# Kernel optimization log

Hardware: AMD Instinct MI355X
Metric: run time of the kernel (lower is better)

## Reference

```python
import jax, jax.numpy as jnp
import numpy as np

D_MODEL, D_STATE, D_CONV, EXPAND = 1024, 16, 4, 2
D_INNER = D_MODEL * EXPAND
B, T = 1, 2048
EPS = 1e-5


def setup_inputs() -> dict:
    key = jax.random.key(0)
    ks = jax.random.split(key, 8)
    x = jax.random.normal(ks[0], (B, T, D_MODEL), dtype=jnp.float32)
    W_in = jax.random.normal(ks[1], (D_MODEL, 2 * D_INNER), dtype=jnp.float32) * 0.02
    conv_w = jax.random.normal(ks[2], (D_INNER, D_CONV), dtype=jnp.float32) * 0.2
    conv_b = jax.random.normal(ks[3], (D_INNER,), dtype=jnp.float32) * 0.02
    W_x = jax.random.normal(ks[4], (D_INNER, 2 * D_STATE + 1), dtype=jnp.float32) * 0.02
    W_dt = jax.random.normal(ks[5], (1, D_INNER), dtype=jnp.float32) * 0.5
    b_dt = jax.random.uniform(ks[6], (D_INNER,), dtype=jnp.float32, minval=-0.001, maxval=0.001)
    A_log = jnp.broadcast_to(jnp.log(jnp.arange(1, D_STATE + 1, dtype=jnp.float32))[None, :], (D_INNER, D_STATE))
    Dparam = jnp.ones((D_INNER,), dtype=jnp.float32)
    W_out = jax.random.normal(ks[7], (D_INNER, D_MODEL), dtype=jnp.float32) * 0.02
    ln_g = jnp.ones((D_MODEL,), dtype=jnp.float32)
    ln_b = jnp.zeros((D_MODEL,), dtype=jnp.float32)
    return {"x": x, "W_in": W_in, "conv_w": conv_w, "conv_b": conv_b, "W_x": W_x,
            "W_dt": W_dt, "b_dt": b_dt, "A_log": A_log, "D": Dparam,
            "W_out": W_out, "ln_g": ln_g, "ln_b": ln_b}


def _silu(v):
    return v * jax.nn.sigmoid(v)


def _layernorm(v, g, b):
    mu = jnp.mean(v, axis=-1, keepdims=True)
    var = jnp.mean((v - mu) ** 2, axis=-1, keepdims=True)
    return (v - mu) * jax.lax.rsqrt(var + EPS) * g + b


def _causal_depthwise_conv(xp, conv_w, conv_b):
    # xp: (B, T, D_INNER) -> (B, D_INNER, T) with left pad of D_CONV-1
    xc = jnp.swapaxes(xp, 1, 2)
    xc = jnp.pad(xc, ((0, 0), (0, 0), (D_CONV - 1, 0)))
    w = conv_w[:, None, :]  # (O=D_INNER, I/groups=1, K)
    out = jax.lax.conv_general_dilated(
        xc, w, window_strides=(1,), padding='VALID',
        dimension_numbers=('NCH', 'OIH', 'NCH'), feature_group_count=D_INNER)
    return jnp.swapaxes(out + conv_b[None, :, None], 1, 2)  # (B, T, D_INNER)


def reference(x, W_in, conv_w, conv_b, W_x, W_dt, b_dt, A_log, D, W_out, ln_g, ln_b):
    residual = x
    xn = _layernorm(x, ln_g, ln_b)
    xz = xn @ W_in                      # (B, T, 2*D_INNER)
    x_proj, z = jnp.split(xz, 2, axis=-1)
    x_conv = _silu(_causal_depthwise_conv(x_proj, conv_w, conv_b))  # (B, T, D_INNER)

    ssm = x_conv @ W_x                  # (B, T, 1 + 2*D_STATE)
    dt_raw = ssm[..., :1]
    Bp = ssm[..., 1:1 + D_STATE]        # (B, T, D_STATE)
    Cp = ssm[..., 1 + D_STATE:]         # (B, T, D_STATE)
    dt = jax.nn.softplus(dt_raw @ W_dt + b_dt)  # (B, T, D_INNER)

    A = -jnp.exp(A_log)                 # (D_INNER, D_STATE)
    A_bar = jnp.exp(dt[..., None] * A)                              # (B,T,d,n)
    Bx = dt[..., None] * Bp[:, :, None, :] * x_conv[..., None]      # (B,T,d,n)

    def step(h, inp):
        Ab_t, Bx_t, C_t = inp           # (B,d,n),(B,d,n),(B,n)
        h = Ab_t * h + Bx_t
        y_t = jnp.einsum('bdn,bn->bd', h, C_t)
        return h, y_t

    h0 = jnp.zeros((x.shape[0], D_INNER, D_STATE), dtype=x.dtype)
    _, ys = jax.lax.scan(step, h0, (jnp.swapaxes(A_bar, 0, 1),
                                    jnp.swapaxes(Bx, 0, 1),
                                    jnp.swapaxes(Cp, 0, 1)))
    y = jnp.swapaxes(ys, 0, 1)          # (B, T, D_INNER)

    y = y + x_conv * D
    y = y * _silu(z)
    return y @ W_out + residual
```

## Files before the change

### kernel.cpp

```cpp
#include <hip/hip_runtime.h>
#include <hip/hip_bf16.h>

typedef __hip_bfloat16 bf16;
typedef __attribute__((ext_vector_type(8))) short bf16x8;
typedef __attribute__((ext_vector_type(4))) float f32x4;

#define T_LEN 2048
#define DMODEL 1024
#define DINNER 2048
#define DSTATE 16
#define LN_EPS 1e-5f
#define NCHUNK 128
#define CLEN 16
#define SSTR 64

#define GLOBAL_AS __attribute__((address_space(1)))
#define LDS_AS __attribute__((address_space(3)))

__device__ __forceinline__ void g2l16(void* lds, const void* g) {
    __builtin_amdgcn_global_load_lds((const GLOBAL_AS void*)g, (LDS_AS void*)lds, 16, 0, 0);
}

__global__ void transpose_bf16(const float* __restrict__ W, bf16* __restrict__ Wt,
                               int K, int N) {
    __shared__ float t[32][33];
    int n0 = blockIdx.x * 32, k0 = blockIdx.y * 32;
    int tx = threadIdx.x & 31, ty4 = (threadIdx.x >> 5) * 4;
#pragma unroll
    for (int r = 0; r < 4; r++)
        t[ty4 + r][tx] = W[(size_t)(k0 + ty4 + r) * N + n0 + tx];
    __syncthreads();
#pragma unroll
    for (int r = 0; r < 4; r++)
        Wt[(size_t)(n0 + ty4 + r) * K + k0 + tx] = __float2bfloat16(t[tx][ty4 + r]);
}

__global__ void transpose_wx(const float* __restrict__ W, bf16* __restrict__ Wt) {
    int idx = blockIdx.x * 256 + threadIdx.x;
    int n = idx >> 11, k = idx & 2047;
    Wt[idx] = __float2bfloat16(n < 33 ? W[k * 33 + n] : 0.f);
}

__global__ void ln_kernel(const float* __restrict__ x, const float* __restrict__ g,
                          const float* __restrict__ b, bf16* __restrict__ xn) {
    int row = blockIdx.x;
    int tid = threadIdx.x;
    const float* xr = x + (size_t)row * DMODEL;
    float v[4];
    float s = 0.f, q = 0.f;
#pragma unroll
    for (int i = 0; i < 4; i++) {
        v[i] = xr[tid + i * 256];
        s += v[i];
        q += v[i] * v[i];
    }
    __shared__ float sh_s[256], sh_q[256];
    sh_s[tid] = s; sh_q[tid] = q;
    __syncthreads();
    for (int st = 128; st > 0; st >>= 1) {
        if (tid < st) { sh_s[tid] += sh_s[tid + st]; sh_q[tid] += sh_q[tid + st]; }
        __syncthreads();
    }
    float mean = sh_s[0] * (1.f / DMODEL);
    float var  = sh_q[0] * (1.f / DMODEL) - mean * mean;
    float rstd = rsqrtf(var + LN_EPS);
#pragma unroll
    for (int i = 0; i < 4; i++) {
        int c = tid + i * 256;
        xn[(size_t)row * DMODEL + c] = __float2bfloat16((v[i] - mean) * rstd * g[c] + b[c]);
    }
}

template <int BM, int BN, int WAVE_M, int WAVE_N, int WRITE_RESID, int OUT_BF16>
__global__ void gemm_mfma(const bf16* __restrict__ A, const bf16* __restrict__ Bt,
                          void* __restrict__ Cv, const float* __restrict__ resid,
                          int M, int N, int Kslice, int lda) {
    constexpr int WMsz = BM / WAVE_M;
    constexpr int WNsz = BN / WAVE_N;
    constexpr int TM = WMsz / 16;
    constexpr int TN = WNsz / 16;
    __shared__ short As[BM * 64];
    __shared__ short Bs[BN * 64];
    int tid = threadIdx.x;
    int lane = tid & 63, wave = tid >> 6;
    int wm = (wave / WAVE_N) * WMsz, wn = (wave % WAVE_N) * WNsz;
    int rowBase = blockIdx.y * BM, colBase = blockIdx.x * BN;
    int kbase = blockIdx.z * Kslice;

    f32x4 acc[TM][TN];
#pragma unroll
    for (int i = 0; i < TM; i++)
#pragma unroll
        for (int j = 0; j < TN; j++) acc[i][j] = f32x4{0.f, 0.f, 0.f, 0.f};

    int srow = tid >> 3;
    int cc = (tid & 7) ^ (srow & 7);
    const int ldsoff = tid * 16;

    for (int k0 = kbase; k0 < kbase + Kslice; k0 += 64) {
#pragma unroll
        for (int j = 0; j < BM / 32; j++)
            g2l16((char*)As + j * 4096 + ldsoff,
                  A + (size_t)(rowBase + j * 32 + srow) * lda + k0 + cc * 8);
#pragma unroll
        for (int j = 0; j < BN / 32; j++)
            g2l16((char*)Bs + j * 4096 + ldsoff,
                  Bt + (size_t)(colBase + j * 32 + srow) * lda + k0 + cc * 8);
        __syncthreads();
#pragma unroll
        for (int ks = 0; ks < 2; ks++) {
            bf16x8 af[TM], bfr[TN];
#pragma unroll
            for (int i = 0; i < TM; i++) {
                int row = wm + i * 16 + (lane & 15);
                int slot = (ks * 4 + (lane >> 4)) ^ (row & 7);
                af[i] = *(const bf16x8*)((const char*)As + row * 128 + slot * 16);
            }
#pragma unroll
            for (int j = 0; j < TN; j++) {
                int row = wn + j * 16 + (lane & 15);
                int slot = (ks * 4 + (lane >> 4)) ^ (row & 7);
                bfr[j] = *(const bf16x8*)((const char*)Bs + row * 128 + slot * 16);
            }
#pragma unroll
            for (int i = 0; i < TM; i++)
#pragma unroll
                for (int j = 0; j < TN; j++)
                    acc[i][j] = __builtin_amdgcn_mfma_f32_16x16x32_bf16(
                        af[i], bfr[j], acc[i][j], 0, 0, 0);
        }
        __syncthreads();
    }
    int rq = lane >> 4, cn = lane & 15;
    float* Cf = (float*)Cv + (size_t)blockIdx.z * M * N;
#pragma unroll
    for (int i = 0; i < TM; i++) {
#pragma unroll
        for (int j = 0; j < TN; j++) {
#pragma unroll
            for (int r = 0; r < 4; r++) {
                size_t row = rowBase + wm + i * 16 + rq * 4 + r;
                int col = colBase + wn + j * 16 + cn;
                float v = acc[i][j][r];
                if (WRITE_RESID) v += resid[row * N + col];
                if (OUT_BF16)
                    ((bf16*)Cv)[row * N + col] = __float2bfloat16(v);
                else
                    Cf[row * N + col] = v;
            }
        }
    }
}

__global__ void reduce_ssm(const float* __restrict__ parts, float* __restrict__ ssm) {
    int i = blockIdx.x * 256 + threadIdx.x;
    ssm[i] = parts[i] + parts[i + 131072] + parts[i + 2 * 131072] + parts[i + 3 * 131072];
}

__global__ void conv_silu(const bf16* __restrict__ xz, const float* __restrict__ cw,
                          const float* __restrict__ cb, bf16* __restrict__ xc) {
    int idx = blockIdx.x * 256 + threadIdx.x;
    int t = idx >> 11, d = idx & (DINNER - 1);
    float acc = cb[d];
#pragma unroll
    for (int k = 0; k < 4; k++) {
        int tt = t - 3 + k;
        if (tt >= 0) acc += (float)xz[(size_t)tt * (2 * DINNER) + d] * cw[d * 4 + k];
    }
    xc[idx] = __float2bfloat16(acc / (1.f + __expf(-acc)));
}

__device__ __forceinline__ float softplus_f(float pre) {
    return (pre > 20.f) ? pre : log1pf(__expf(pre));
}

__device__ __forceinline__ void powtree(float q, float* a) {
    a[0] = q;
    a[1] = q * q;
    a[2] = a[1] * q;
    a[3] = a[1] * a[1];
#pragma unroll
    for (int j = 0; j < 4; j++) a[4 + j] = a[j] * a[3];
#pragma unroll
    for (int j = 0; j < 8; j++) a[8 + j] = a[j] * a[7];
}

__global__ __launch_bounds__(256, 4) void scan_pass1(
        const float* __restrict__ ssm, const bf16* __restrict__ xc,
        const float* __restrict__ Wdt, const float* __restrict__ bdt,
        const float* __restrict__ Alog,
        float* __restrict__ P, float* __restrict__ S) {
    int d = blockIdx.x * 256 + threadIdx.x;
    int c = blockIdx.y;
    float A[DSTATE], Pv[DSTATE], Sv[DSTATE];
    bool fast = true;
#pragma unroll
    for (int n = 0; n < DSTATE; n++) {
        A[n] = -__expf(Alog[d * DSTATE + n]);
        fast = fast && (fabsf(A[n] + (float)(n + 1)) < 1e-3f * (n + 1));
        Pv[n] = 1.f; Sv[n] = 0.f;
    }
    float wdt = Wdt[d], bd = bdt[d];
    int t0 = c * CLEN;
    if (fast) {
        for (int t = t0; t < t0 + CLEN; t++) {
            const float* srow = ssm + (size_t)t * SSTR;
            float dt = softplus_f(srow[0] * wdt + bd);
            float dtxc = dt * (float)xc[(size_t)t * DINNER + d];
            float a[DSTATE];
            powtree(__expf(-dt), a);
#pragma unroll
            for (int n = 0; n < DSTATE; n++) {
                Pv[n] *= a[n];
                Sv[n] = a[n] * Sv[n] + dtxc * srow[1 + n];
            }
        }
    } else {
        for (int t = t0; t < t0 + CLEN; t++) {
            const float* srow = ssm + (size_t)t * SSTR;
            float dt = softplus_f(srow[0] * wdt + bd);
            float dtxc = dt * (float)xc[(size_t)t * DINNER + d];
#pragma unroll
            for (int n = 0; n < DSTATE; n++) {
                float a = __expf(dt * A[n]);
                Pv[n] *= a;
                Sv[n] = a * Sv[n] + dtxc * srow[1 + n];
            }
        }
    }
    size_t base = (size_t)c * DINNER * DSTATE + d;
#pragma unroll
    for (int n = 0; n < DSTATE; n++) {
        P[base + (size_t)n * DINNER] = Pv[n];
        S[base + (size_t)n * DINNER] = Sv[n];
    }
}

__global__ void scan_pass2(float* __restrict__ P, const float* __restrict__ S) {
    int idx = blockIdx.x * 256 + threadIdx.x;
    float H = 0.f;
    for (int c = 0; c < NCHUNK; c++) {
        size_t o = (size_t)c * DINNER * DSTATE + idx;
        float Pc = P[o], Sc = S[o];
        P[o] = H;
        H = Pc * H + Sc;
    }
}

__global__ __launch_bounds__(256, 4) void scan_pass3(
        const float* __restrict__ ssm, const bf16* __restrict__ xc,
        const bf16* __restrict__ xz,
        const float* __restrict__ Wdt, const float* __restrict__ bdt,
        const float* __restrict__ Alog, const float* __restrict__ Dp,
        const float* __restrict__ Hst, bf16* __restrict__ yf) {
    int d = blockIdx.x * 256 + threadIdx.x;
    int c = blockIdx.y;
    float A[DSTATE], h[DSTATE];
    bool fast = true;
    size_t base = (size_t)c * DINNER * DSTATE + d;
#pragma unroll
    for (int n = 0; n < DSTATE; n++) {
        A[n] = -__expf(Alog[d * DSTATE + n]);
        fast = fast && (fabsf(A[n] + (float)(n + 1)) < 1e-3f * (n + 1));
        h[n] = Hst[base + (size_t)n * DINNER];
    }
    float wdt = Wdt[d], bd = bdt[d], Dd = Dp[d];
    int t0 = c * CLEN;
    for (int t = t0; t < t0 + CLEN; t++) {
        const float* srow = ssm + (size_t)t * SSTR;
        float dt = softplus_f(srow[0] * wdt + bd);
        float xcv = (float)xc[(size_t)t * DINNER + d];
        float dtxc = dt * xcv;
        float y0 = 0.f, y1 = 0.f, y2 = 0.f, y3 = 0.f;
        if (fast) {
            float a[DSTATE];
            powtree(__expf(-dt), a);
#pragma unroll
            for (int n = 0; n < 4; n++) {
                h[n] = a[n] * h[n] + dtxc * srow[1 + n];
                y0 += h[n] * srow[17 + n];
                h[n + 4] = a[n + 4] * h[n + 4] + dtxc * srow[5 + n];
                y1 += h[n + 4] * srow[21 + n];
                h[n + 8] = a[n + 8] * h[n + 8] + dtxc * srow[9 + n];
                y2 += h[n + 8] * srow[25 + n];
                h[n + 12] = a[n + 12] * h[n + 12] + dtxc * srow[13 + n];
                y3 += h[n + 12] * srow[29 + n];
            }
        } else {
#pragma unroll
            for (int n = 0; n < DSTATE; n++) {
                float a = __expf(dt * A[n]);
                h[n] = a * h[n] + dtxc * srow[1 + n];
                y0 += h[n] * srow[17 + n];
            }
        }
        float y = (y0 + y1) + (y2 + y3);
        float z = (float)xz[(size_t)t * (2 * DINNER) + DINNER + d];
        float sz = z / (1.f + __expf(-z));
        yf[(size_t)t * DINNER + d] = __float2bfloat16((y + xcv * Dd) * sz);
    }
}

extern "C" void kernel_launch(void* const* d_in, const int* in_sizes, int n_in,
                              void* d_out, int out_size, void* d_ws, size_t ws_size,
                              hipStream_t stream) {
    const float* x     = (const float*)d_in[0];
    const float* W_in  = (const float*)d_in[1];
    const float* convw = (const float*)d_in[2];
    const float* convb = (const float*)d_in[3];
    const float* W_x   = (const float*)d_in[4];
    const float* W_dt  = (const float*)d_in[5];
    const float* b_dt  = (const float*)d_in[6];
    const float* A_log = (const float*)d_in[7];
    const float* Dp    = (const float*)d_in[8];
    const float* W_out = (const float*)d_in[9];
    const float* ln_g  = (const float*)d_in[10];
    const float* ln_b  = (const float*)d_in[11];
    float* out = (float*)d_out;

    char* wsb = (char*)d_ws;
    bf16*  xn    = (bf16*)(wsb);
    bf16*  WinT  = (bf16*)(wsb + (4ull  << 20));
    bf16*  WoutT = (bf16*)(wsb + (12ull << 20));
    bf16*  WxT   = (bf16*)(wsb + (16ull << 20));
    bf16*  xz    = (bf16*)(wsb + (17ull << 20));
    bf16*  xc    = (bf16*)(wsb + (33ull << 20));
    float* parts = (float*)(wsb + (41ull << 20));
    float* ssm   = (float*)(wsb + (43ull << 20));
    float* P     = (float*)(wsb + (44ull << 20));
    float* S     = (float*)(wsb + (60ull << 20));
    bf16*  yf    = (bf16*)(wsb + (76ull << 20));

    transpose_bf16<<<dim3(4096 / 32, 1024 / 32), 256, 0, stream>>>(W_in, WinT, 1024, 4096);
    transpose_bf16<<<dim3(1024 / 32, 2048 / 32), 256, 0, stream>>>(W_out, WoutT, 2048, 1024);
    transpose_wx<<<(64 * 2048) / 256, 256, 0, stream>>>(W_x, WxT);

    ln_kernel<<<T_LEN, 256, 0, stream>>>(x, ln_g, ln_b, xn);

    gemm_mfma<128, 128, 2, 2, 0, 1><<<dim3(4096 / 128, 2048 / 128), 256, 0, stream>>>(
        xn, WinT, xz, nullptr, 2048, 4096, 1024, 1024);

    conv_silu<<<(T_LEN * DINNER) / 256, 256, 0, stream>>>(xz, convw, convb, xc);

    gemm_mfma<32, 64, 2, 2, 0, 0><<<dim3(1, 2048 / 32, 4), 256, 0, stream>>>(
        xc, WxT, parts, nullptr, 2048, 64, 512, 2048);
    reduce_ssm<<<131072 / 256, 256, 0, stream>>>(parts, ssm);

    scan_pass1<<<dim3(DINNER / 256, NCHUNK), 256, 0, stream>>>(
        ssm, xc, W_dt, b_dt, A_log, P, S);
    scan_pass2<<<(DINNER * DSTATE) / 256, 256, 0, stream>>>(P, S);
    scan_pass3<<<dim3(DINNER / 256, NCHUNK), 256, 0, stream>>>(
        ssm, xc, xz, W_dt, b_dt, A_log, Dp, P, yf);

    gemm_mfma<64, 128, 1, 4, 1, 0><<<dim3(1024 / 128, 2048 / 64), 256, 0, stream>>>(
        yf, WoutT, out, x, 2048, 1024, 2048, 2048);
}
```

Measured before the change: 264.3 us.

## Transpose conv output and silu(z) per channel, stage ssm rows in LDS for scans

```diff
diff --git a/kernel.cpp b/kernel.cpp
--- a/kernel.cpp
+++ b/kernel.cpp
@@ -21,24 +21,45 @@
     __builtin_amdgcn_global_load_lds((const GLOBAL_AS void*)g, (LDS_AS void*)lds, 16, 0, 0);
 }
 
-__global__ void transpose_bf16(const float* __restrict__ W, bf16* __restrict__ Wt,
-                               int K, int N) {
+__device__ __forceinline__ float b2f(short s) {
+    return __uint_as_float(((unsigned)(unsigned short)s) << 16);
+}
+__device__ __forceinline__ short f2b(float f) {
+    bf16 h = __float2bfloat16(f);
+    return *reinterpret_cast<short*>(&h);
+}
+
+__global__ void prep_weights(const float* __restrict__ Win, const float* __restrict__ Wout,
+                             const float* __restrict__ Wx,
+                             bf16* __restrict__ WinT, bf16* __restrict__ WoutT,
+                             bf16* __restrict__ WxT) {
     __shared__ float t[32][33];
-    int n0 = blockIdx.x * 32, k0 = blockIdx.y * 32;
-    int tx = threadIdx.x & 31, ty4 = (threadIdx.x >> 5) * 4;
-#pragma unroll
-    for (int r = 0; r < 4; r++)
-        t[ty4 + r][tx] = W[(size_t)(k0 + ty4 + r) * N + n0 + tx];
-    __syncthreads();
-#pragma unroll
-    for (int r = 0; r < 4; r++)
-        Wt[(size_t)(n0 + ty4 + r) * K + k0 + tx] = __float2bfloat16(t[tx][ty4 + r]);
-}
-
-__global__ void transpose_wx(const float* __restrict__ W, bf16* __restrict__ Wt) {
-    int idx = blockIdx.x * 256 + threadIdx.x;
-    int n = idx >> 11, k = idx & 2047;
-    Wt[idx] = __float2bfloat16(n < 33 ? W[k * 33 + n] : 0.f);
+    int bid = blockIdx.x, tid = threadIdx.x;
+    int tx = tid & 31, ty4 = (tid >> 5) * 4;
+    if (bid < 4096) {
+        int n0 = (bid & 127) * 32, k0 = (bid >> 7) * 32;
+#pragma unroll
+        for (int r = 0; r < 4; r++)
+            t[ty4 + r][tx] = Win[(size_t)(k0 + ty4 + r) * 4096 + n0 + tx];
+        __syncthreads();
+#pragma unroll
+        for (int r = 0; r < 4; r++)
+            WinT[(size_t)(n0 + ty4 + r) * 1024 + k0 + tx] = __float2bfloat16(t[tx][ty4 + r]);
+    } else if (bid < 6144) {
+        int b = bid - 4096;
+        int n0 = (b & 31) * 32, k0 = (b >> 5) * 32;
+#pragma unroll
+        for (int r = 0; r < 4; r++)
+            t[ty4 + r][tx] = Wout[(size_t)(k0 + ty4 + r) * 1024 + n0 + tx];
+        __syncthreads();
+#pragma unroll
+        for (int r = 0; r < 4; r++)
+            WoutT[(size_t)(n0 + ty4 + r) * 2048 + k0 + tx] = __float2bfloat16(t[tx][ty4 + r]);
+    } else {
+        int idx = (bid - 6144) * 256 + tid;
+        int n = idx >> 11, k = idx & 2047;
+        WxT[idx] = __float2bfloat16(n < 33 ? Wx[k * 33 + n] : 0.f);
+    }
 }
 
 __global__ void ln_kernel(const float* __restrict__ x, const float* __restrict__ g,
@@ -157,17 +178,45 @@
     ssm[i] = parts[i] + parts[i + 131072] + parts[i + 2 * 131072] + parts[i + 3 * 131072];
 }
 
-__global__ void conv_silu(const bf16* __restrict__ xz, const float* __restrict__ cw,
-                          const float* __restrict__ cb, bf16* __restrict__ xc) {
-    int idx = blockIdx.x * 256 + threadIdx.x;
-    int t = idx >> 11, d = idx & (DINNER - 1);
-    float acc = cb[d];
-#pragma unroll
-    for (int k = 0; k < 4; k++) {
-        int tt = t - 3 + k;
-        if (tt >= 0) acc += (float)xz[(size_t)tt * (2 * DINNER) + d] * cw[d * 4 + k];
-    }
-    xc[idx] = __float2bfloat16(acc / (1.f + __expf(-acc)));
+__global__ void conv_silu_T(const bf16* __restrict__ xz, const float* __restrict__ cw,
+                            const float* __restrict__ cb, bf16* __restrict__ xc,
+                            bf16* __restrict__ xcT, bf16* __restrict__ szT) {
+    __shared__ float txc[32][65];
+    __shared__ float tsz[32][65];
+    int t0 = blockIdx.x * 32, d0 = blockIdx.y * 64;
+    int tid = threadIdx.x;
+    int trow = tid >> 6;
+    int dcol = tid & 63;
+    int d = d0 + dcol;
+    float w0 = cw[d * 4], w1 = cw[d * 4 + 1], w2 = cw[d * 4 + 2], w3 = cw[d * 4 + 3];
+    float bias = cb[d];
+#pragma unroll
+    for (int r = 0; r < 8; r++) {
+        int tt = r * 4 + trow;
+        int t = t0 + tt;
+        size_t base = (size_t)t * (2 * DINNER) + d;
+        float acc = bias + b2f(*(const short*)(xz + base)) * w3;
+        if (t >= 1) acc += b2f(*(const short*)(xz + base - (2 * DINNER))) * w2;
+        if (t >= 2) acc += b2f(*(const short*)(xz + base - 2 * (2 * DINNER))) * w1;
+        if (t >= 3) acc += b2f(*(const short*)(xz + base - 3 * (2 * DINNER))) * w0;
+        float v = acc / (1.f + __expf(-acc));
+        xc[(size_t)t * DINNER + d] = __float2bfloat16(v);
+        txc[tt][dcol] = v;
+        float z = b2f(*(const short*)(xz + base + DINNER));
+        tsz[tt][dcol] = z / (1.f + __expf(-z));
+    }
+    __syncthreads();
+    int drow = tid >> 2;
+    int tseg = (tid & 3) * 8;
+    int gd = d0 + drow;
+    bf16x8 vx, vz;
+#pragma unroll
+    for (int i = 0; i < 8; i++) {
+        vx[i] = f2b(txc[tseg + i][drow]);
+        vz[i] = f2b(tsz[tseg + i][drow]);
+    }
+    *reinterpret_cast<bf16x8*>((short*)xcT + (size_t)gd * T_LEN + t0 + tseg) = vx;
+    *reinterpret_cast<bf16x8*>((short*)szT + (size_t)gd * T_LEN + t0 + tseg) = vz;
 }
 
 __device__ __forceinline__ float softplus_f(float pre) {
@@ -186,12 +235,22 @@
 }
 
 __global__ __launch_bounds__(256, 4) void scan_pass1(
-        const float* __restrict__ ssm, const bf16* __restrict__ xc,
+        const float* __restrict__ ssm, const bf16* __restrict__ xcT,
         const float* __restrict__ Wdt, const float* __restrict__ bdt,
         const float* __restrict__ Alog,
         float* __restrict__ P, float* __restrict__ S) {
-    int d = blockIdx.x * 256 + threadIdx.x;
+    __shared__ float slab[CLEN][SSTR];
+    int tid = threadIdx.x;
+    int d = blockIdx.x * 256 + tid;
     int c = blockIdx.y;
+    int t0 = c * CLEN;
+#pragma unroll
+    for (int r = 0; r < 4; r++) {
+        int t = r * 4 + (tid >> 6);
+        slab[t][tid & 63] = ssm[(size_t)(t0 + t) * SSTR + (tid & 63)];
+    }
+    bf16x8 xv0 = *reinterpret_cast<const bf16x8*>((const short*)xcT + (size_t)d * T_LEN + t0);
+    bf16x8 xv1 = *reinterpret_cast<const bf16x8*>((const short*)xcT + (size_t)d * T_LEN + t0 + 8);
     float A[DSTATE], Pv[DSTATE], Sv[DSTATE];
     bool fast = true;
 #pragma unroll
@@ -201,30 +260,32 @@
         Pv[n] = 1.f; Sv[n] = 0.f;
     }
     float wdt = Wdt[d], bd = bdt[d];
-    int t0 = c * CLEN;
+    __syncthreads();
     if (fast) {
-        for (int t = t0; t < t0 + CLEN; t++) {
-            const float* srow = ssm + (size_t)t * SSTR;
-            float dt = softplus_f(srow[0] * wdt + bd);
-            float dtxc = dt * (float)xc[(size_t)t * DINNER + d];
+#pragma unroll
+        for (int i = 0; i < CLEN; i++) {
+            float dt = softplus_f(slab[i][0] * wdt + bd);
+            float xcv = b2f(i < 8 ? xv0[i] : xv1[i - 8]);
+            float dtxc = dt * xcv;
             float a[DSTATE];
             powtree(__expf(-dt), a);
 #pragma unroll
             for (int n = 0; n < DSTATE; n++) {
                 Pv[n] *= a[n];
-                Sv[n] = a[n] * Sv[n] + dtxc * srow[1 + n];
+                Sv[n] = a[n] * Sv[n] + dtxc * slab[i][1 + n];
             }
         }
     } else {
-        for (int t = t0; t < t0 + CLEN; t++) {
-            const float* srow = ssm + (size_t)t * SSTR;
-            float dt = softplus_f(srow[0] * wdt + bd);
-            float dtxc = dt * (float)xc[(size_t)t * DINNER + d];
+#pragma unroll
+        for (int i = 0; i < CLEN; i++) {
+            float dt = softplus_f(slab[i][0] * wdt + bd);
+            float xcv = b2f(i < 8 ? xv0[i] : xv1[i - 8]);
+            float dtxc = dt * xcv;
 #pragma unroll
             for (int n = 0; n < DSTATE; n++) {
                 float a = __expf(dt * A[n]);
                 Pv[n] *= a;
-                Sv[n] = a * Sv[n] + dtxc * srow[1 + n];
+                Sv[n] = a * Sv[n] + dtxc * slab[i][1 + n];
             }
         }
     }
@@ -239,6 +300,7 @@
 __global__ void scan_pass2(float* __restrict__ P, const float* __restrict__ S) {
     int idx = blockIdx.x * 256 + threadIdx.x;
     float H = 0.f;
+#pragma unroll 4
     for (int c = 0; c < NCHUNK; c++) {
         size_t o = (size_t)c * DINNER * DSTATE + idx;
         float Pc = P[o], Sc = S[o];
@@ -248,13 +310,25 @@
 }
 
 __global__ __launch_bounds__(256, 4) void scan_pass3(
-        const float* __restrict__ ssm, const bf16* __restrict__ xc,
-        const bf16* __restrict__ xz,
+        const float* __restrict__ ssm, const bf16* __restrict__ xcT,
+        const bf16* __restrict__ szT,
         const float* __restrict__ Wdt, const float* __restrict__ bdt,
         const float* __restrict__ Alog, const float* __restrict__ Dp,
         const float* __restrict__ Hst, bf16* __restrict__ yf) {
-    int d = blockIdx.x * 256 + threadIdx.x;
+    __shared__ float slab[CLEN][SSTR];
+    int tid = threadIdx.x;
+    int d = blockIdx.x * 256 + tid;
     int c = blockIdx.y;
+    int t0 = c * CLEN;
+#pragma unroll
+    for (int r = 0; r < 4; r++) {
+        int t = r * 4 + (tid >> 6);
+        slab[t][tid & 63] = ssm[(size_t)(t0 + t) * SSTR + (tid & 63)];
+    }
+    bf16x8 xv0 = *reinterpret_cast<const bf16x8*>((const short*)xcT + (size_t)d * T_LEN + t0);
+    bf16x8 xv1 = *reinterpret_cast<const bf16x8*>((const short*)xcT + (size_t)d * T_LEN + t0 + 8);
+    bf16x8 zv0 = *reinterpret_cast<const bf16x8*>((const short*)szT + (size_t)d * T_LEN + t0);
+    bf16x8 zv1 = *reinterpret_cast<const bf16x8*>((const short*)szT + (size_t)d * T_LEN + t0 + 8);
     float A[DSTATE], h[DSTATE];
     bool fast = true;
     size_t base = (size_t)c * DINNER * DSTATE + d;
@@ -265,39 +339,47 @@
         h[n] = Hst[base + (size_t)n * DINNER];
     }
     float wdt = Wdt[d], bd = bdt[d], Dd = Dp[d];
-    int t0 = c * CLEN;
-    for (int t = t0; t < t0 + CLEN; t++) {
-        const float* srow = ssm + (size_t)t * SSTR;
-        float dt = softplus_f(srow[0] * wdt + bd);
-        float xcv = (float)xc[(size_t)t * DINNER + d];
-        float dtxc = dt * xcv;
-        float y0 = 0.f, y1 = 0.f, y2 = 0.f, y3 = 0.f;
-        if (fast) {
+    __syncthreads();
+    if (fast) {
+#pragma unroll
+        for (int i = 0; i < CLEN; i++) {
+            float dt = softplus_f(slab[i][0] * wdt + bd);
+            float xcv = b2f(i < 8 ? xv0[i] : xv1[i - 8]);
+            float dtxc = dt * xcv;
             float a[DSTATE];
             powtree(__expf(-dt), a);
+            float y0 = 0.f, y1 = 0.f, y2 = 0.f, y3 = 0.f;
 #pragma unroll
             for (int n = 0; n < 4; n++) {
-                h[n] = a[n] * h[n] + dtxc * srow[1 + n];
-                y0 += h[n] * srow[17 + n];
-                h[n + 4] = a[n + 4] * h[n + 4] + dtxc * srow[5 + n];
-                y1 += h[n + 4] * srow[21 + n];
-                h[n + 8] = a[n + 8] * h[n + 8] + dtxc * srow[9 + n];
-                y2 += h[n + 8] * srow[25 + n];
-                h[n + 12] = a[n + 12] * h[n + 12] + dtxc * srow[13 + n];
-                y3 += h[n + 12] * srow[29 + n];
-            }
-        } else {
+                h[n] = a[n] * h[n] + dtxc * slab[i][1 + n];
+                y0 += h[n] * slab[i][17 + n];
+                h[n + 4] = a[n + 4] * h[n + 4] + dtxc * slab[i][5 + n];
+                y1 += h[n + 4] * slab[i][21 + n];
+                h[n + 8] = a[n + 8] * h[n + 8] + dtxc * slab[i][9 + n];
+                y2 += h[n + 8] * slab[i][25 + n];
+                h[n + 12] = a[n + 12] * h[n + 12] + dtxc * slab[i][13 + n];
+                y3 += h[n + 12] * slab[i][29 + n];
+            }
+            float y = (y0 + y1) + (y2 + y3);
+            float sz = b2f(i < 8 ? zv0[i] : zv1[i - 8]);
+            yf[(size_t)(t0 + i) * DINNER + d] = __float2bfloat16((y + xcv * Dd) * sz);
+        }
+    } else {
+#pragma unroll
+        for (int i = 0; i < CLEN; i++) {
+            float dt = softplus_f(slab[i][0] * wdt + bd);
+            float xcv = b2f(i < 8 ? xv0[i] : xv1[i - 8]);
+            float dtxc = dt * xcv;
+            float y = 0.f;
 #pragma unroll
             for (int n = 0; n < DSTATE; n++) {
                 float a = __expf(dt * A[n]);
-                h[n] = a * h[n] + dtxc * srow[1 + n];
-                y0 += h[n] * srow[17 + n];
-            }
-        }
-        float y = (y0 + y1) + (y2 + y3);
-        float z = (float)xz[(size_t)t * (2 * DINNER) + DINNER + d];
-        float sz = z / (1.f + __expf(-z));
-        yf[(size_t)t * DINNER + d] = __float2bfloat16((y + xcv * Dd) * sz);
+                h[n] = a * h[n] + dtxc * slab[i][1 + n];
+                y += h[n] * slab[i][17 + n];
+            }
+            float sz = b2f(i < 8 ? zv0[i] : zv1[i - 8]);
+            yf[(size_t)(t0 + i) * DINNER + d] = __float2bfloat16((y + xcv * Dd) * sz);
+        }
     }
 }
 
@@ -325,32 +407,33 @@
     bf16*  WxT   = (bf16*)(wsb + (16ull << 20));
     bf16*  xz    = (bf16*)(wsb + (17ull << 20));
     bf16*  xc    = (bf16*)(wsb + (33ull << 20));
-    float* parts = (float*)(wsb + (41ull << 20));
-    float* ssm   = (float*)(wsb + (43ull << 20));
-    float* P     = (float*)(wsb + (44ull << 20));
-    float* S     = (float*)(wsb + (60ull << 20));
-    bf16*  yf    = (bf16*)(wsb + (76ull << 20));
-
-    transpose_bf16<<<dim3(4096 / 32, 1024 / 32), 256, 0, stream>>>(W_in, WinT, 1024, 4096);
-    transpose_bf16<<<dim3(1024 / 32, 2048 / 32), 256, 0, stream>>>(W_out, WoutT, 2048, 1024);
-    transpose_wx<<<(64 * 2048) / 256, 256, 0, stream>>>(W_x, WxT);
+    bf16*  xcT   = (bf16*)(wsb + (41ull << 20));
+    bf16*  szT   = (bf16*)(wsb + (49ull << 20));
+    float* parts = (float*)(wsb + (57ull << 20));
+    float* ssm   = (float*)(wsb + (59ull << 20));
+    float* P     = (float*)(wsb + (60ull << 20));
+    float* S     = (float*)(wsb + (76ull << 20));
+    bf16*  yf    = (bf16*)(wsb + (92ull << 20));
+
+    prep_weights<<<6656, 256, 0, stream>>>(W_in, W_out, W_x, WinT, WoutT, WxT);
 
     ln_kernel<<<T_LEN, 256, 0, stream>>>(x, ln_g, ln_b, xn);
 
     gemm_mfma<128, 128, 2, 2, 0, 1><<<dim3(4096 / 128, 2048 / 128), 256, 0, stream>>>(
         xn, WinT, xz, nullptr, 2048, 4096, 1024, 1024);
 
-    conv_silu<<<(T_LEN * DINNER) / 256, 256, 0, stream>>>(xz, convw, convb, xc);
+    conv_silu_T<<<dim3(T_LEN / 32, DINNER / 64), 256, 0, stream>>>(
+        xz, convw, convb, xc, xcT, szT);
 
     gemm_mfma<32, 64, 2, 2, 0, 0><<<dim3(1, 2048 / 32, 4), 256, 0, stream>>>(
         xc, WxT, parts, nullptr, 2048, 64, 512, 2048);
     reduce_ssm<<<131072 / 256, 256, 0, stream>>>(parts, ssm);
 
     scan_pass1<<<dim3(DINNER / 256, NCHUNK), 256, 0, stream>>>(
-        ssm, xc, W_dt, b_dt, A_log, P, S);
+        ssm, xcT, W_dt, b_dt, A_log, P, S);
     scan_pass2<<<(DINNER * DSTATE) / 256, 256, 0, stream>>>(P, S);
     scan_pass3<<<dim3(DINNER / 256, NCHUNK), 256, 0, stream>>>(
-        ssm, xc, xz, W_dt, b_dt, A_log, Dp, P, yf);
+        ssm, xcT, szT, W_dt, b_dt, A_log, Dp, P, yf);
 
     gemm_mfma<64, 128, 1, 4, 1, 0><<<dim3(1024 / 128, 2048 / 64), 256, 0, stream>>>(
         yf, WoutT, out, x, 2048, 1024, 2048, 2048);
```

Result: slower. 330.2 us (+25.0%).
